# Performance work log

Hardware: AMD Instinct MI355X
Metric: run time of the kernel (lower is better)

## Reference

```python
import jax, jax.numpy as jnp
import numpy as np

N_EMBED = 1024
N_HEAD = 16
HEAD_SIZE = N_EMBED // N_HEAD  # 64
SEQ = 2048
BATCH = 2
EPS = 1e-5


def setup_inputs() -> dict:
    key = jax.random.key(0)
    ks = jax.random.split(key, 16)
    s = lambda fan_in: 1.0 / np.sqrt(fan_in)
    d, h, hs, f = N_EMBED, N_HEAD, HEAD_SIZE, 4 * N_EMBED
    return {
        "x": jax.random.normal(ks[0], (BATCH, SEQ, d), dtype=jnp.float32),
        # per-head QKV projections (no bias), stacked over heads: [H, D, hs]
        "wq": jax.random.normal(ks[1], (h, d, hs), dtype=jnp.float32) * s(d),
        "wk": jax.random.normal(ks[2], (h, d, hs), dtype=jnp.float32) * s(d),
        "wv": jax.random.normal(ks[3], (h, d, hs), dtype=jnp.float32) * s(d),
        "w_proj": jax.random.normal(ks[4], (d, d), dtype=jnp.float32) * s(d),
        "b_proj": jnp.zeros((d,), dtype=jnp.float32),
        "w1": jax.random.normal(ks[5], (d, f), dtype=jnp.float32) * s(d),
        "b1": jnp.zeros((f,), dtype=jnp.float32),
        "w2": jax.random.normal(ks[6], (f, d), dtype=jnp.float32) * s(f),
        "b2": jnp.zeros((d,), dtype=jnp.float32),
        "g1": jnp.ones((d,), dtype=jnp.float32),
        "be1": jnp.zeros((d,), dtype=jnp.float32),
        "g2": jnp.ones((d,), dtype=jnp.float32),
        "be2": jnp.zeros((d,), dtype=jnp.float32),
    }


def _layer_norm(x, gamma, beta):
    mu = jnp.mean(x, axis=-1, keepdims=True)
    var = jnp.mean(jnp.square(x - mu), axis=-1, keepdims=True)
    return (x - mu) * jax.lax.rsqrt(var + EPS) * gamma + beta


def reference(x, wq, wk, wv, w_proj, b_proj, w1, b1, w2, b2, g1, be1, g2, be2):
    B, S, D = x.shape
    # per-head projections (vectorized over heads): [B, H, S, hs]
    q = jnp.einsum("bsd,hdk->bhsk", x, wq)
    k = jnp.einsum("bsd,hdk->bhsk", x, wk)
    v = jnp.einsum("bsd,hdk->bhsk", x, wv)
    scale = HEAD_SIZE ** -0.5
    scores = jnp.einsum("bhsk,bhtk->bhst", q, k) * scale  # [B,H,S,S]
    causal = jnp.tril(jnp.ones((S, S), dtype=bool))
    scores = jnp.where(causal, scores, -jnp.inf)
    w = jax.nn.softmax(scores, axis=-1)  # dropout=0 -> identity
    attn = jnp.einsum("bhst,bhtk->bhsk", w, v)  # [B,H,S,hs]
    # concat heads (head-major ordering matches torch.cat over heads)
    attn = attn.transpose(0, 2, 1, 3).reshape(B, S, D)
    y = attn @ w_proj + b_proj
    x = _layer_norm(x + y, g1, be1)
    y = jax.nn.relu(x @ w1 + b1) @ w2 + b2
    x = _layer_norm(x + y, g2, be2)
    return x
```

## Files before the change

kernel.cpp:

```cpp
#include <hip/hip_runtime.h>


typedef unsigned short u16;
typedef unsigned int u32;
typedef __attribute__((ext_vector_type(8))) short bf16x8;
typedef __attribute__((ext_vector_type(4))) float f32x4;
typedef __attribute__((ext_vector_type(2))) u32 u32x2;
typedef __attribute__((ext_vector_type(4))) _Float16 f16x4;

#define MFMA16(a, b, c) __builtin_amdgcn_mfma_f32_16x16x32_bf16(a, b, c, 0, 0, 0)
#define MFMAH(a, b, c) __builtin_amdgcn_mfma_f32_16x16x16f16(a, b, c, 0, 0, 0)

__device__ __forceinline__ u16 f2b(float f) {
  unsigned int u = __builtin_bit_cast(unsigned int, f);
  u = (u + 0x7fffu + ((u >> 16) & 1u)) >> 16;
  return (u16)u;
}

__device__ __forceinline__ void gload_lds16(const u16* g, u16* l) {
  __builtin_amdgcn_global_load_lds((const __attribute__((address_space(1))) void*)g,
                                   (__attribute__((address_space(3))) void*)l, 16, 0, 0);
}

__device__ __forceinline__ u32 pkrtz(float lo, float hi) {
  return __builtin_bit_cast(u32, __builtin_amdgcn_cvt_pkrtz(lo, hi));
}

__device__ __forceinline__ f16x4 pack4h(float a, float b, float c, float d) {
  u32x2 r = {pkrtz(a, b), pkrtz(c, d)};
  return __builtin_bit_cast(f16x4, r);
}

__device__ __forceinline__ u16 f2h(float v) {
  return __builtin_bit_cast(u16, (_Float16)v);
}


__global__ __launch_bounds__(256) void pack_all(
    const float* __restrict__ x, const float* __restrict__ wq,
    const float* __restrict__ wk, const float* __restrict__ wv,
    const float* __restrict__ wp, const float* __restrict__ w1,
    const float* __restrict__ w2, u16* __restrict__ Xbf, u16* __restrict__ WqkvT,
    u16* __restrict__ WprojT, u16* __restrict__ W1T, u16* __restrict__ W2T) {
  int bid = blockIdx.x;
  int t = threadIdx.x;
  if (bid >= 12288) {
    size_t i = ((size_t)(bid - 12288) * 256 + t) * 4;
    float4 v = *(const float4*)(x + i);
    Xbf[i + 0] = f2b(v.x);
    Xbf[i + 1] = f2b(v.y);
    Xbf[i + 2] = f2b(v.z);
    Xbf[i + 3] = f2b(v.w);
    return;
  }
  __shared__ float tile[32][33];
  int tx = t & 31, ty = t >> 5;
  const float* src;
  u16* dst;
  int R, C, r0, c0;
  float scale = 1.0f;
  if (bid < 3072) {
    int z = bid >> 6, q = bid & 63;
    int p = z >> 4, h = z & 15;
    src = (p == 0 ? wq : (p == 1 ? wk : wv)) + (size_t)h * 1024 * 64;
    scale = (p == 0) ? 0.1803368801f : 1.0f;
    dst = WqkvT + (size_t)(p * 1024 + h * 64) * 1024;
    R = 1024; C = 64;
    c0 = (q & 1) * 32; r0 = (q >> 1) * 32;
  } else if (bid < 4096) {
    int q = bid - 3072;
    src = wp; dst = WprojT; R = 1024; C = 1024;
    c0 = (q & 31) * 32; r0 = (q >> 5) * 32;
  } else if (bid < 8192) {
    int q = bid - 4096;
    src = w1; dst = W1T; R = 1024; C = 4096;
    c0 = (q & 127) * 32; r0 = (q >> 7) * 32;
  } else {
    int q = bid - 8192;
    src = w2; dst = W2T; R = 4096; C = 1024;
    c0 = (q & 31) * 32; r0 = (q >> 5) * 32;
  }
#pragma unroll
  for (int i = 0; i < 4; ++i)
    tile[ty + i * 8][tx] = src[(size_t)(r0 + ty + i * 8) * C + c0 + tx];
  __syncthreads();
#pragma unroll
  for (int i = 0; i < 4; ++i)
    dst[(size_t)(c0 + ty + i * 8) * R + r0 + tx] = f2b(tile[tx][ty + i * 8] * scale);
}


template <int MODE>
__global__ __launch_bounds__(256, 4) void gemm_bf16(const u16* __restrict__ A,
                                                    const u16* __restrict__ Bt, int M,
                                                    int N, int Kc, int lda,
                                                    const float* __restrict__ bias,
                                                    u16* __restrict__ outB, int ldc,
                                                    u16* __restrict__ vtg) {
  constexpr int BM = 128, BN = 128, BK = 64;
  constexpr int IM = 4, JN = 4;
  __shared__ u16 As[BM * BK];
  __shared__ u16 Bs[BN * BK];
  int t = threadIdx.x;
  int m0 = blockIdx.x * BM, n0 = blockIdx.y * BN;
  int kb = blockIdx.z * Kc;
  int lane = t & 63, wid = t >> 6;
  int wm = (wid >> 1) * 64, wn = (wid & 1) * 64;
  int m16 = lane & 15, quad = lane >> 4;
  int sw = m16 & 7;

  f32x4 acc[IM][JN] = {};

  for (int k0 = kb; k0 < kb + Kc; k0 += BK) {
    __syncthreads();
#pragma unroll
    for (int i = 0; i < 4; ++i) {
      int S = i * 256 + t;
      int row = S >> 3, c = S & 7;
      gload_lds16(&A[(size_t)(m0 + row) * lda + k0 + (c ^ (row & 7)) * 8],
                  &As[(i * 256 + wid * 64) * 8]);
    }
#pragma unroll
    for (int i = 0; i < 4; ++i) {
      int S = i * 256 + t;
      int row = S >> 3, c = S & 7;
      gload_lds16(&Bt[(size_t)(n0 + row) * lda + k0 + (c ^ (row & 7)) * 8],
                  &Bs[(i * 256 + wid * 64) * 8]);
    }
    __syncthreads();
#pragma unroll
    for (int kk = 0; kk < 2; ++kk) {
      bf16x8 af[IM], bfr[JN];
      int slot = (kk * 4 + quad) ^ sw;
#pragma unroll
      for (int i = 0; i < IM; ++i)
        af[i] = *(const bf16x8*)&As[(wm + i * 16 + m16) * BK + slot * 8];
#pragma unroll
      for (int j = 0; j < JN; ++j)
        bfr[j] = *(const bf16x8*)&Bs[(wn + j * 16 + m16) * BK + slot * 8];
#pragma unroll
      for (int i = 0; i < IM; ++i)
#pragma unroll
        for (int j = 0; j < JN; ++j) acc[i][j] = MFMA16(af[i], bfr[j], acc[i][j]);
    }
  }

  if (MODE == 3 && n0 >= 2048) {
#pragma unroll
    for (int i = 0; i < IM; ++i)
#pragma unroll
      for (int j = 0; j < JN; ++j) {
        int dg = n0 + wn + j * 16 + m16 - 2048;
        int hh = dg >> 6, dd = dg & 63;
        int token = m0 + wm + i * 16 + quad * 4;
        int bb = token >> 11, tt = token & 2047;
        u32x2 pv = {pkrtz(acc[i][j][0], acc[i][j][1]),
                    pkrtz(acc[i][j][2], acc[i][j][3])};
        *(u32x2*)&vtg[(((size_t)bb * 16 + hh) * 64 + dd) * 2048 + tt] = pv;
      }
    return;
  }

  u16* pb = (MODE == 4) ? outB + (size_t)blockIdx.z * M * N : outB;
#pragma unroll
  for (int i = 0; i < IM; ++i)
#pragma unroll
    for (int j = 0; j < JN; ++j) {
      int col = n0 + wn + j * 16 + m16;
      float bv = (MODE == 1) ? bias[col] : 0.0f;
#pragma unroll
      for (int r = 0; r < 4; ++r) {
        int row = m0 + wm + i * 16 + quad * 4 + r;
        float v = acc[i][j][r];
        if (MODE == 1) {
          v += bv;
          v = v > 0.0f ? v : 0.0f;
          pb[(size_t)row * ldc + col] = f2b(v);
        } else if (MODE == 4) {
          pb[(size_t)row * ldc + col] = f2h(v);
        } else {
          pb[(size_t)row * ldc + col] = f2b(v);
        }
      }
    }
}


__constant__ unsigned char R_QB[30] = {
    5, 11, 11, 10, 10, 15, 15, 4, 9, 9, 13, 14, 14, 14, 15,
    8, 8, 12, 12, 13, 13, 3, 7, 7, 12, 6, 6, 2, 1, 0};
__constant__ unsigned char R_K0[30] = {
    0, 0, 12, 0, 11, 0, 11, 0, 0, 10, 0, 0, 10, 20, 22,
    0, 9, 0, 9, 10, 19, 0, 0, 8, 18, 0, 7, 0, 0, 0};
__constant__ unsigned char R_NIT[30] = {
    12, 12, 12, 11, 11, 11, 11, 10, 10, 10, 10, 10, 10, 10, 10,
    9, 9, 9, 9, 9, 9, 8, 8, 8, 8, 7, 7, 6, 4, 2};
__constant__ unsigned char R_ST[30] = {
    255, 10, 11, 8, 9, 21, 22, 255, 6, 7, 15, 18, 19, 20, 23,
    4, 5, 12, 13, 16, 17, 255, 2, 3, 14, 0, 1, 255, 255, 255};
__constant__ unsigned char CB_BASE[10] = {0, 2, 4, 6, 8, 10, 12, 15, 18, 21};

__global__ __launch_bounds__(256) void attn_part(const u16* __restrict__ qk,
                                                 const u16* __restrict__ vtg,
                                                 u16* __restrict__ attn_out,
                                                 u16* __restrict__ opart,
                                                 float2* __restrict__ ml) {
  int rank = blockIdx.x >> 5, bh = blockIdx.x & 31;
  int qb = R_QB[rank];
  int k_start = R_K0[rank] * 64;
  int iters = R_NIT[rank];
  int st = R_ST[rank];
  int b = bh >> 4, h = bh & 15;

  int t = threadIdx.x, lane = t & 63, w = t >> 6;
  int m16 = lane & 15, quad = lane >> 4;
  int wq0 = qb * 128 + w * 32;

  __shared__ u16 Ks[2][64 * 64];
  __shared__ u16 Vs[2][64 * 64];

  bf16x8 qa[2][2];
#pragma unroll
  for (int qs = 0; qs < 2; ++qs) {
    const u16* qp = qk + (size_t)(b * 2048 + wq0 + qs * 16 + m16) * 2048 + h * 64;
    qa[qs][0] = *(const bf16x8*)&qp[quad * 8];
    qa[qs][1] = *(const bf16x8*)&qp[32 + quad * 8];
  }

  f32x4 oT[2][4] = {};
  f32x4 lacc[2] = {};

  int row0 = t >> 3, c0 = t & 7;
  int row1 = 32 + row0;
  const u16* kbase = qk + (size_t)(b * 2048) * 2048 + 1024 + h * 64;
  const u16* vbase = vtg + ((size_t)(b * 16 + h) * 64) * 2048;
  int sw = m16 & 7;

#define STAGE_ASYNC(T0, BUF)                                                        \
  {                                                                                 \
    gload_lds16(&kbase[(size_t)((T0) + row0) * 2048 + (c0 ^ (row0 & 7)) * 8],       \
                &Ks[BUF][(w * 64) * 8]);                                            \
    gload_lds16(&kbase[(size_t)((T0) + row1) * 2048 + (c0 ^ (row1 & 7)) * 8],       \
                &Ks[BUF][(256 + w * 64) * 8]);                                      \
    gload_lds16(&vbase[(size_t)row0 * 2048 + (T0) + (c0 ^ (row0 & 7)) * 8],         \
                &Vs[BUF][(w * 64) * 8]);                                            \
    gload_lds16(&vbase[(size_t)row1 * 2048 + (T0) + (c0 ^ (row1 & 7)) * 8],         \
                &Vs[BUF][(256 + w * 64) * 8]);                                      \
  }

  STAGE_ASYNC(k_start, 0);
  __syncthreads();

  for (int it = 0; it < iters; ++it) {
    int t0 = k_start + it * 64;
    int cur = it & 1;
    if (it + 1 < iters) STAGE_ASYNC(t0 + 64, !cur);

    if (t0 <= wq0 + 31) {
      f32x4 sv[2][4];
      __builtin_amdgcn_s_setprio(1);
#pragma unroll
      for (int ts = 0; ts < 4; ++ts) {
        bf16x8 ka0 = *(const bf16x8*)&Ks[cur][(ts * 16 + m16) * 64 + (quad ^ sw) * 8];
        bf16x8 ka1 =
            *(const bf16x8*)&Ks[cur][(ts * 16 + m16) * 64 + ((4 + quad) ^ sw) * 8];
#pragma unroll
        for (int qs = 0; qs < 2; ++qs) {
          f32x4 a = {};
          a = MFMA16(ka0, qa[qs][0], a);
          a = MFMA16(ka1, qa[qs][1], a);
          sv[qs][ts] = a;
        }
      }
      __builtin_amdgcn_s_setprio(0);
      if (t0 + 63 > wq0) {
#pragma unroll
        for (int qs = 0; qs < 2; ++qs)
#pragma unroll
          for (int ts = 0; ts < 4; ++ts)
#pragma unroll
            for (int rr = 0; rr < 4; ++rr) {
              int key = t0 + ts * 16 + quad * 4 + rr;
              if (key > wq0 + qs * 16 + m16) sv[qs][ts][rr] = -3e38f;
            }
      }
      f16x4 pf[2][4];
#pragma unroll
      for (int qs = 0; qs < 2; ++qs)
#pragma unroll
        for (int ts = 0; ts < 4; ++ts) {
          float p0 = exp2f(sv[qs][ts][0] - 8.0f);
          float p1 = exp2f(sv[qs][ts][1] - 8.0f);
          float p2 = exp2f(sv[qs][ts][2] - 8.0f);
          float p3 = exp2f(sv[qs][ts][3] - 8.0f);
          lacc[qs][0] += p0;
          lacc[qs][1] += p1;
          lacc[qs][2] += p2;
          lacc[qs][3] += p3;
          pf[qs][ts] = pack4h(p0, p1, p2, p3);
        }
      __builtin_amdgcn_s_setprio(1);
#pragma unroll
      for (int ts = 0; ts < 4; ++ts)
#pragma unroll
        for (int ds = 0; ds < 4; ++ds) {
          f16x4 av = __builtin_bit_cast(
              f16x4, *(const u32x2*)&Vs[cur][(ds * 16 + m16) * 64 +
                                             (((ts * 2 + (quad >> 1)) ^ sw) * 8) +
                                             (quad & 1) * 4]);
          oT[0][ds] = MFMAH(av, pf[0][ts], oT[0][ds]);
          oT[1][ds] = MFMAH(av, pf[1][ts], oT[1][ds]);
        }
      __builtin_amdgcn_s_setprio(0);
    }
    __syncthreads();
  }
#undef STAGE_ASYNC

  if (st == 255) {
#pragma unroll
    for (int qs = 0; qs < 2; ++qs) {
      float ls = lacc[qs][0] + lacc[qs][1] + lacc[qs][2] + lacc[qs][3];
      ls += __shfl_xor(ls, 16);
      ls += __shfl_xor(ls, 32);
      float rl = 1.0f / ls;
      int q = wq0 + qs * 16 + m16;
#pragma unroll
      for (int ds = 0; ds < 4; ++ds) {
        f32x4 o = oT[qs][ds];
        u32x2 ov = {(u32)f2b(o[0] * rl) | ((u32)f2b(o[1] * rl) << 16),
                    (u32)f2b(o[2] * rl) | ((u32)f2b(o[3] * rl) << 16)};
        *(u32x2*)&attn_out[(size_t)(b * 2048 + q) * 1024 + h * 64 + ds * 16 +
                           quad * 4] = ov;
      }
    }
  } else {
    size_t sb = ((size_t)st * 32 + bh) * 128;
#pragma unroll
    for (int qs = 0; qs < 2; ++qs) {
      float ls = lacc[qs][0] + lacc[qs][1] + lacc[qs][2] + lacc[qs][3];
      ls += __shfl_xor(ls, 16);
      ls += __shfl_xor(ls, 32);
      int qloc = w * 32 + qs * 16 + m16;
#pragma unroll
      for (int ds = 0; ds < 4; ++ds) {
        f32x4 o = oT[qs][ds];
        u32x2 ov = {pkrtz(o[0], o[1]), pkrtz(o[2], o[3])};
        *(u32x2*)&opart[(sb + qloc) * 64 + ds * 16 + quad * 4] = ov;
      }
      if (quad == 0) ml[sb + qloc] = make_float2(0.0f, ls);
    }
  }
}

__global__ __launch_bounds__(256) void attn_comb(const u16* __restrict__ opart,
                                                 const float2* __restrict__ ml,
                                                 u16* __restrict__ attn_out) {
  int qb = 6 + blockIdx.x, bh = blockIdx.y;
  int b = bh >> 4, h = bh & 15;
  int nseg = (qb < 12) ? 2 : 3;
  int base = CB_BASE[qb - 6];
  int t = threadIdx.x;
  int q = t >> 1, dh = (t & 1) * 32;

  float lsum = 0.0f;
  for (int s = 0; s < nseg; ++s)
    lsum += ml[((size_t)(base + s) * 32 + bh) * 128 + q].y;
  float rl = 1.0f / lsum;

  constexpr size_t SLOT = (size_t)32 * 128 * 64;
  const u16* orow[3];
  for (int s = 0; s < nseg; ++s)
    orow[s] = opart + (size_t)(base + s) * SLOT + ((size_t)bh * 128 + q) * 64 + dh;

  size_t oout = (size_t)(b * 2048 + qb * 128 + q) * 1024 + h * 64 + dh;
#pragma unroll 2
  for (int dd = 0; dd < 32; dd += 4) {
    float o0 = 0, o1 = 0, o2 = 0, o3 = 0;
    for (int s = 0; s < nseg; ++s) {
      f16x4 hv = __builtin_bit_cast(f16x4, *(const u32x2*)&orow[s][dd]);
      o0 += (float)hv[0];
      o1 += (float)hv[1];
      o2 += (float)hv[2];
      o3 += (float)hv[3];
    }
    u32x2 ov = {(u32)f2b(o0 * rl) | ((u32)f2b(o1 * rl) << 16),
                (u32)f2b(o2 * rl) | ((u32)f2b(o3 * rl) << 16)};
    *(u32x2*)&attn_out[oout + dd] = ov;
  }
}


__global__ __launch_bounds__(256) void ln_comb(const u16* __restrict__ parts, int np,
                                               const float* __restrict__ bias,
                                               const float* __restrict__ resid,
                                               const float* __restrict__ g,
                                               const float* __restrict__ be,
                                               float* __restrict__ outF,
                                               u16* __restrict__ outB) {
  int row = blockIdx.x;
  int t = threadIdx.x;
  size_t off = (size_t)row * 1024 + t * 4;
  float4 bv4 = *(const float4*)(bias + t * 4);
  float a0 = bv4.x, a1 = bv4.y, a2 = bv4.z, a3 = bv4.w;
  for (int c = 0; c < np; ++c) {
    f16x4 hv =
        __builtin_bit_cast(f16x4, *(const u32x2*)&parts[(size_t)c * 4096 * 1024 + off]);
    a0 += (float)hv[0];
    a1 += (float)hv[1];
    a2 += (float)hv[2];
    a3 += (float)hv[3];
  }
  float4 rv = *(const float4*)(resid + off);
  a0 += rv.x;
  a1 += rv.y;
  a2 += rv.z;
  a3 += rv.w;

  float s = a0 + a1 + a2 + a3;
  float sq = a0 * a0 + a1 * a1 + a2 * a2 + a3 * a3;
#pragma unroll
  for (int d = 1; d < 64; d <<= 1) {
    s += __shfl_xor(s, d);
    sq += __shfl_xor(sq, d);
  }
  __shared__ float red[8];
  int lane = t & 63, wid = t >> 6;
  if (lane == 0) {
    red[wid] = s;
    red[4 + wid] = sq;
  }
  __syncthreads();
  s = red[0] + red[1] + red[2] + red[3];
  sq = red[4] + red[5] + red[6] + red[7];
  float mu = s * (1.0f / 1024.0f);
  float var = sq * (1.0f / 1024.0f) - mu * mu;
  float rstd = rsqrtf(var + 1e-5f);
  float4 gv = *(const float4*)(g + t * 4);
  float4 bev = *(const float4*)(be + t * 4);
  float o0 = (a0 - mu) * rstd * gv.x + bev.x;
  float o1 = (a1 - mu) * rstd * gv.y + bev.y;
  float o2 = (a2 - mu) * rstd * gv.z + bev.z;
  float o3 = (a3 - mu) * rstd * gv.w + bev.w;
  if (outF) {
    float4 ov = {o0, o1, o2, o3};
    *(float4*)(outF + off) = ov;
  }
  if (outB) {
    outB[off + 0] = f2b(o0);
    outB[off + 1] = f2b(o1);
    outB[off + 2] = f2b(o2);
    outB[off + 3] = f2b(o3);
  }
}


extern "C" void kernel_launch(void* const* d_in, const int* in_sizes, int n_in,
                              void* d_out, int out_size, void* d_ws, size_t ws_size,
                              hipStream_t stream) {
  const float* x = (const float*)d_in[0];
  const float* wq = (const float*)d_in[1];
  const float* wk = (const float*)d_in[2];
  const float* wv = (const float*)d_in[3];
  const float* w_proj = (const float*)d_in[4];
  const float* b_proj = (const float*)d_in[5];
  const float* w1 = (const float*)d_in[6];
  const float* b1 = (const float*)d_in[7];
  const float* w2 = (const float*)d_in[8];
  const float* b2 = (const float*)d_in[9];
  const float* g1 = (const float*)d_in[10];
  const float* be1 = (const float*)d_in[11];
  const float* g2 = (const float*)d_in[12];
  const float* be2 = (const float*)d_in[13];
  float* out = (float*)d_out;

  const int M = 4096;
  char* w = (char*)d_ws;
  u16* Xbf = (u16*)w;        w += (size_t)M * 1024 * 2;
  u16* WqkvT = (u16*)w;      w += (size_t)3072 * 1024 * 2;
  u16* WprojT = (u16*)w;     w += (size_t)1024 * 1024 * 2;
  u16* W1T = (u16*)w;        w += (size_t)4096 * 1024 * 2;
  u16* X1b = (u16*)w;        w += (size_t)M * 1024 * 2;
  u16* W2T = (u16*)w;        w += (size_t)1024 * 4096 * 2;
  u16* QK = (u16*)w;         w += (size_t)M * 2048 * 2;
  u16* Vtg = (u16*)w;        w += (size_t)2 * 16 * 64 * 2048 * 2;
  u16* Attn = (u16*)w;       w += (size_t)M * 1024 * 2;
  float* X1f = (float*)w;    w += (size_t)M * 1024 * 4;

  u16* Pdown = Xbf;
  u16* Pproj = QK;
  u16* Hbuf = QK;
  u16* Opart = (u16*)X1f;
  float2* Ml = (float2*)((char*)d_ws + (size_t)4 * 1024 * 1024);

  pack_all<<<16384, 256, 0, stream>>>(x, wq, wk, wv, w_proj, w1, w2, Xbf, WqkvT,
                                      WprojT, W1T, W2T);

  gemm_bf16<3><<<dim3(32, 24, 1), 256, 0, stream>>>(Xbf, WqkvT, M, 3072, 1024, 1024,
                                                    nullptr, QK, 2048, Vtg);

  attn_part<<<960, 256, 0, stream>>>(QK, Vtg, Attn, Opart, Ml);
  attn_comb<<<dim3(10, 32), 256, 0, stream>>>(Opart, Ml, Attn);

  gemm_bf16<4><<<dim3(32, 8, 2), 256, 0, stream>>>(Attn, WprojT, M, 1024, 512, 1024,
                                                   nullptr, Pproj, 1024, nullptr);
  ln_comb<<<M, 256, 0, stream>>>(Pproj, 2, b_proj, x, g1, be1, X1f, X1b);

  gemm_bf16<1><<<dim3(32, 32, 1), 256, 0, stream>>>(X1b, W1T, M, 4096, 1024, 1024, b1,
                                                    Hbuf, 4096, nullptr);

  gemm_bf16<4><<<dim3(32, 8, 4), 256, 0, stream>>>(Hbuf, W2T, M, 1024, 1024, 4096,
                                                   nullptr, Pdown, 1024, nullptr);
  ln_comb<<<M, 256, 0, stream>>>(Pdown, 4, b2, X1f, g2, be2, out, nullptr);
}
```

Measured before the change: 329.3 us.

## Add 256x256-tile 8-wave pipelined GEMM kernel for FFN matmuls

Adds a new 512-thread GEMM kernel with 256x256 output tiles. It uses double-buffered LDS staging through global_load_lds, XOR-swizzled layout, and loads for the next k-steps interleaved across the four compute sub-phases. The two FFN GEMMs (up projection with bias+ReLU, split-K down projection) now use it instead of the 128-tile kernel. The goal is more operand reuse per LDS byte and better overlap of memory traffic with MFMA work. The cost is larger LDS use, more registers per thread (32 accumulators), and fewer blocks in the grid (256 per GEMM), which may leave CUs underfilled.

```diff
diff --git a/kernel.cpp b/kernel.cpp
--- a/kernel.cpp
+++ b/kernel.cpp
@@ -186,6 +186,158 @@
 }
 
 
+template <int MODE>
+__global__ __launch_bounds__(512) void gemm8(const u16* __restrict__ A,
+                                             const u16* __restrict__ Bt, int M, int N,
+                                             int Kc, int lda,
+                                             const float* __restrict__ bias,
+                                             u16* __restrict__ outB, int ldc) {
+  __shared__ __align__(16) u16 As[2][2][128 * 64];
+  __shared__ __align__(16) u16 Bs[2][2][128 * 64];
+  int t = threadIdx.x;
+  int lane = t & 63, wid = t >> 6;
+  int m16 = lane & 15, quad = lane >> 4, sw = m16 & 7;
+  int wr = wid >> 2, wc = wid & 3;
+  int m0 = blockIdx.x * 256, n0 = blockIdx.y * 256;
+  int kb = blockIdx.z * Kc;
+  int NT = Kc >> 6;
+
+  int ahalf = t >> 8;
+  int at = t & 255;
+  int aw = wid & 3;
+
+  f32x4 acc[8][4] = {};
+
+#define STAGE_B(bf, bh, kt)                                                        \
+  {                                                                                \
+    _Pragma("unroll") for (int l = 0; l < 2; ++l) {                                \
+      int slot = l * 512 + t;                                                      \
+      int row = slot >> 3, c = slot & 7;                                           \
+      gload_lds16(&Bt[(size_t)(n0 + (bh)*128 + row) * lda + kb + (kt)*64 +         \
+                      (c ^ (row & 7)) * 8],                                        \
+                  &Bs[bf][bh][(l * 512 + wid * 64) * 8]);                          \
+    }                                                                              \
+  }
+
+#define STAGE_A(bf, qp, kt)                                                        \
+  {                                                                                \
+    _Pragma("unroll") for (int l = 0; l < 2; ++l) {                                \
+      int slot = l * 256 + at;                                                     \
+      int row = slot >> 3, c = slot & 7;                                           \
+      int lrow = (qp)*64 + row;                                                    \
+      gload_lds16(&A[(size_t)(m0 + ahalf * 128 + lrow) * lda + kb + (kt)*64 +      \
+                     (c ^ (row & 7)) * 8],                                         \
+                  &As[bf][ahalf][((qp)*512 + l * 256 + aw * 64) * 8]);             \
+    }                                                                              \
+  }
+
+#define FENCE asm volatile("" ::: "memory")
+
+  STAGE_B(0, 0, 0);
+  STAGE_B(0, 1, 0);
+  STAGE_A(0, 0, 0);
+  STAGE_A(0, 1, 0);
+  if (NT > 1) {
+    STAGE_B(1, 0, 1);
+    STAGE_B(1, 1, 1);
+    STAGE_A(1, 0, 1);
+  }
+  asm volatile("s_waitcnt vmcnt(0)" ::: "memory");
+  FENCE;
+  __builtin_amdgcn_s_barrier();
+  FENCE;
+
+  const u16* Ah[2] = {As[0][wr], As[1][wr]};
+  const u16* Bh[2] = {Bs[0][wc >> 1], Bs[1][wc >> 1]};
+  int brow0 = (wc & 1) * 64;
+
+  for (int kt = 0; kt < NT; ++kt) {
+    int buf = kt & 1;
+    const u16* Abase = Ah[buf];
+    const u16* Bbase = Bh[buf];
+
+    bf16x8 bfrag[4][2];
+#pragma unroll
+    for (int j = 0; j < 4; ++j)
+#pragma unroll
+      for (int kk = 0; kk < 2; ++kk)
+        bfrag[j][kk] = *(const bf16x8*)&Bbase[(brow0 + j * 16 + m16) * 64 +
+                                              (((kk * 4 + quad)) ^ sw) * 8];
+
+#pragma unroll
+    for (int qd = 0; qd < 4; ++qd) {
+      bf16x8 af[2][2];
+#pragma unroll
+      for (int mi = 0; mi < 2; ++mi)
+#pragma unroll
+        for (int kk = 0; kk < 2; ++kk)
+          af[mi][kk] = *(const bf16x8*)&Abase[(qd * 32 + mi * 16 + m16) * 64 +
+                                              ((kk * 4 + quad) ^ sw) * 8];
+      if (qd == 0) {
+        if (kt + 1 < NT) STAGE_A(!buf, 1, kt + 1);
+      } else if (qd == 1) {
+        if (kt + 2 < NT) STAGE_B(buf, 0, kt + 2);
+      } else if (qd == 2) {
+        if (kt + 2 < NT) STAGE_B(buf, 1, kt + 2);
+      } else {
+        if (kt + 2 < NT) STAGE_A(buf, 0, kt + 2);
+      }
+      FENCE;
+      __builtin_amdgcn_s_barrier();
+      FENCE;
+      asm volatile("s_waitcnt lgkmcnt(0)" ::: "memory");
+      __builtin_amdgcn_sched_barrier(0);
+      __builtin_amdgcn_s_setprio(1);
+#pragma unroll
+      for (int mi = 0; mi < 2; ++mi)
+#pragma unroll
+        for (int j = 0; j < 4; ++j)
+#pragma unroll
+          for (int kk = 0; kk < 2; ++kk)
+            acc[qd * 2 + mi][j] = MFMA16(af[mi][kk], bfrag[j][kk], acc[qd * 2 + mi][j]);
+      __builtin_amdgcn_s_setprio(0);
+      if (qd < 3) {
+        FENCE;
+        __builtin_amdgcn_s_barrier();
+        FENCE;
+      } else {
+        if (kt + 2 < NT)
+          asm volatile("s_waitcnt vmcnt(6)" ::: "memory");
+        else
+          asm volatile("s_waitcnt vmcnt(0)" ::: "memory");
+        FENCE;
+        __builtin_amdgcn_s_barrier();
+        FENCE;
+      }
+    }
+  }
+
+  u16* pb = (MODE == 4) ? outB + (size_t)blockIdx.z * M * N : outB;
+#pragma unroll
+  for (int mf = 0; mf < 8; ++mf)
+#pragma unroll
+    for (int j = 0; j < 4; ++j) {
+      int col = n0 + wc * 64 + j * 16 + m16;
+      float bv = (MODE == 1) ? bias[col] : 0.0f;
+#pragma unroll
+      for (int r = 0; r < 4; ++r) {
+        int row = m0 + wr * 128 + mf * 16 + quad * 4 + r;
+        float v = acc[mf][j][r];
+        if (MODE == 1) {
+          v += bv;
+          v = v > 0.0f ? v : 0.0f;
+          pb[(size_t)row * ldc + col] = f2b(v);
+        } else {
+          pb[(size_t)row * ldc + col] = f2h(v);
+        }
+      }
+    }
+#undef STAGE_B
+#undef STAGE_A
+#undef FENCE
+}
+
+
 __constant__ unsigned char R_QB[30] = {
     5, 11, 11, 10, 10, 15, 15, 4, 9, 9, 13, 14, 14, 14, 15,
     8, 8, 12, 12, 13, 13, 3, 7, 7, 12, 6, 6, 2, 1, 0};
@@ -506,10 +658,10 @@
                                                    nullptr, Pproj, 1024, nullptr);
   ln_comb<<<M, 256, 0, stream>>>(Pproj, 2, b_proj, x, g1, be1, X1f, X1b);
 
-  gemm_bf16<1><<<dim3(32, 32, 1), 256, 0, stream>>>(X1b, W1T, M, 4096, 1024, 1024, b1,
-                                                    Hbuf, 4096, nullptr);
-
-  gemm_bf16<4><<<dim3(32, 8, 4), 256, 0, stream>>>(Hbuf, W2T, M, 1024, 1024, 4096,
-                                                   nullptr, Pdown, 1024, nullptr);
+  gemm8<1><<<dim3(16, 16, 1), 512, 0, stream>>>(X1b, W1T, M, 4096, 1024, 1024, b1,
+                                                Hbuf, 4096);
+
+  gemm8<4><<<dim3(16, 4, 4), 512, 0, stream>>>(Hbuf, W2T, M, 1024, 1024, 4096,
+                                               nullptr, Pdown, 1024);
   ln_comb<<<M, 256, 0, stream>>>(Pdown, 4, b2, X1f, g2, be2, out, nullptr);
 }
```

Measured after the change: 392.0 us. 1.19x slower.
